# Performance work log

Measured on AMD Instinct MI355X. Metric: run time of the kernel, lower is better.

The kernel has to match this reference:

```python
import jax, jax.numpy as jnp
import numpy as np

B, S, D, H = 2, 2048, 1024, 16
HD = D // H  # head_dim = 64

def setup_inputs() -> dict:
    key = jax.random.key(0)
    ks = jax.random.split(key, 10)
    s = 1.0 / np.sqrt(D)
    return {
        "hidden_states": jax.random.normal(ks[0], (B, S, D), jnp.float32),
        "attention_mask": jnp.ones((B, S), jnp.float32),
        "q_w": jax.random.uniform(ks[1], (D, D), jnp.float32, -s, s),
        "q_b": jax.random.uniform(ks[2], (D,), jnp.float32, -s, s),
        "k_w": jax.random.uniform(ks[3], (D, D), jnp.float32, -s, s),
        "k_b": jax.random.uniform(ks[4], (D,), jnp.float32, -s, s),
        "v_w": jax.random.uniform(ks[5], (D, D), jnp.float32, -s, s),
        "v_b": jax.random.uniform(ks[6], (D,), jnp.float32, -s, s),
        "o_w": jax.random.uniform(ks[7], (D, D), jnp.float32, -s, s),
        "o_b": jax.random.uniform(ks[8], (D,), jnp.float32, -s, s),
    }

def reference(hidden_states, attention_mask, q_w, q_b, k_w, k_b, v_w, v_b, o_w, o_b):
    scale = HD ** -0.5
    # projections; torch Linear: x @ W^T + b. Here weights stored as (D, D) used directly.
    q = hidden_states @ q_w + q_b  # [B,S,D]
    k = hidden_states @ k_w + k_b
    v = hidden_states @ v_w + v_b
    # split heads -> [B,H,S,HD]
    q = q.reshape(B, S, H, HD).transpose(0, 2, 1, 3)
    k = k.reshape(B, S, H, HD).transpose(0, 2, 1, 3)
    v = v.reshape(B, S, H, HD).transpose(0, 2, 1, 3)
    scores = jnp.einsum('bhqd,bhkd->bhqk', q, k) * scale  # [B,H,S,S]
    # additive mask from 2D [B,S] mask (1=keep, 0=mask)
    scores = scores + (1.0 - attention_mask)[:, None, None, :] * -10000.0
    attn = jax.nn.softmax(scores, axis=-1)
    ctx = jnp.einsum('bhqk,bhkd->bhqd', attn, v)  # [B,H,S,HD]
    ctx = ctx.transpose(0, 2, 1, 3).reshape(B, S, D)
    return ctx @ o_w + o_b
```

## Files before the change

kernel.cpp:

```cpp
#include <hip/hip_runtime.h>
#include <hip/hip_bf16.h>

#define B_ 2
#define S_ 2048
#define D_ 1024
#define H_ 16
#define HD_ 64

#define QSCALE 0.18033688f
#define MLOG2E 14426.950408f

#define EXP2(x) __builtin_amdgcn_exp2f(x)

typedef __attribute__((ext_vector_type(8))) short bf16x8;
typedef __attribute__((ext_vector_type(4))) short short4v;
typedef __attribute__((ext_vector_type(4))) float floatx4;
typedef __attribute__((ext_vector_type(16))) float f32x16;

static __device__ __forceinline__ short f2bf(float f) {
  union { float f; unsigned int i; } c; c.f = f;
  unsigned int r = c.i + 0x7FFFu + ((c.i >> 16) & 1u);
  return (short)(r >> 16);
}

static __device__ __forceinline__ int cvtpk_bf16(float a, float b) {
  int r;
  asm("v_cvt_pk_bf16_f32 %0, %1, %2" : "=v"(r) : "v"(a), "v"(b));
  return r;
}
static __device__ __forceinline__ void swap32(int& a, int& b) {
  asm("v_permlane32_swap_b32 %0, %1" : "+v"(a), "+v"(b));
}

static __device__ __forceinline__ void gld_lds16(const void* g, void* l) {
  __builtin_amdgcn_global_load_lds(
      (const __attribute__((address_space(1))) unsigned int*)g,
      (__attribute__((address_space(3))) unsigned int*)l, 16, 0, 0);
}

__global__ __launch_bounds__(256)
void prep(const float* __restrict__ w0, const float* __restrict__ w1,
          const float* __restrict__ w2, const float* __restrict__ w3,
          const float* __restrict__ hs, short* __restrict__ WT,
          short* __restrict__ Xb) {
  const int z = blockIdx.z;
  if (z < 4) {
    __shared__ short t[64][65];
    const float* src = z == 0 ? w0 : z == 1 ? w1 : z == 2 ? w2 : w3;
    short* dst = WT + (size_t)z * D_ * D_;
    const int tx = threadIdx.x & 63, ty = threadIdx.x >> 6;
    const int r0 = blockIdx.y * 64, c0 = blockIdx.x * 64;
    for (int r = ty; r < 64; r += 4)
      t[r][tx] = f2bf(src[(size_t)(r0 + r) * D_ + c0 + tx]);
    __syncthreads();
    for (int r = ty; r < 64; r += 4)
      dst[(size_t)(c0 + r) * D_ + r0 + tx] = t[tx][r];
  } else {
    const int bid = blockIdx.y * 16 + blockIdx.x;
    const float4* in4 = (const float4*)hs;
    short4v* out4 = (short4v*)Xb;
#pragma unroll
    for (int i = 0; i < 16; i++) {
      const int idx = bid * 4096 + i * 256 + threadIdx.x;
      const float4 v = in4[idx];
      short4v o;
      o[0] = f2bf(v.x); o[1] = f2bf(v.y); o[2] = f2bf(v.z); o[3] = f2bf(v.w);
      out4[idx] = o;
    }
  }
}

__global__ __launch_bounds__(256, 2)
void gemm_qkv(const short* __restrict__ X, const short* __restrict__ WT,
              const float* __restrict__ qb, const float* __restrict__ kb,
              const float* __restrict__ vb,
              short* __restrict__ Qo, short* __restrict__ Ko,
              short* __restrict__ Vt) {
  __shared__ __align__(16) short As[128 * 32];
  __shared__ __align__(16) short Bs[128 * 32];
  const int tid = threadIdx.x;
  const int wave = tid >> 6, lane = tid & 63;
  const int col = lane & 15, quad = lane >> 4;
  const int m0 = blockIdx.x * 128;
  const int nt = blockIdx.y;
  const int widx = nt >> 3;
  const int n1 = (nt & 7) * 128;
  const short* Bsrc = WT + (size_t)widx * D_ * D_ + (size_t)n1 * D_;
  const int b = m0 >> 11;

  const int srow = tid >> 2;
  const int skcol = (tid & 3) * 8;
  const short* ga = X + (size_t)(m0 + srow) * D_ + skcol;
  const short* gb = Bsrc + (size_t)srow * D_ + skcol;
  short* la = As + tid * 8;
  short* lb = Bs + tid * 8;

  floatx4 acc[4][4];
#pragma unroll
  for (int i = 0; i < 4; i++)
#pragma unroll
    for (int j = 0; j < 4; j++) acc[i][j] = floatx4{0.f, 0.f, 0.f, 0.f};

  if (widx < 2) {
    const int wseq = (wave >> 1) * 64;
    const int wfeat = (wave & 1) * 64;
    for (int k0 = 0; k0 < D_; k0 += 32) {
      gld_lds16(ga, la);
      gld_lds16(ga + 64 * D_, la + 2048);
      gld_lds16(gb, lb);
      gld_lds16(gb + 64 * D_, lb + 2048);
      ga += 32; gb += 32;
      __syncthreads();
      bf16x8 xf[4], wf[4];
#pragma unroll
      for (int j = 0; j < 4; j++)
        xf[j] = *(const bf16x8*)(As + (wseq + j * 16 + col) * 32 + quad * 8);
#pragma unroll
      for (int i = 0; i < 4; i++)
        wf[i] = *(const bf16x8*)(Bs + (wfeat + i * 16 + col) * 32 + quad * 8);
#pragma unroll
      for (int i = 0; i < 4; i++)
#pragma unroll
        for (int j = 0; j < 4; j++)
          acc[i][j] = __builtin_amdgcn_mfma_f32_16x16x32_bf16(wf[i], xf[j],
                                                              acc[i][j], 0, 0, 0);
      __syncthreads();
    }
    const float* bias = widx == 0 ? qb : kb;
    short* dst = widx == 0 ? Qo : Ko;
    const float scale = widx == 0 ? QSCALE : 1.0f;
#pragma unroll
    for (int i = 0; i < 4; i++) {
      const int nf = n1 + wfeat + i * 16 + quad * 4;
      const int h = nf >> 6, hd = nf & 63;
      const float4 bv = *(const float4*)(bias + nf);
#pragma unroll
      for (int j = 0; j < 4; j++) {
        const int s = (m0 + wseq + j * 16 + col) & (S_ - 1);
        short4v pk;
        pk[0] = f2bf((acc[i][j][0] + bv.x) * scale);
        pk[1] = f2bf((acc[i][j][1] + bv.y) * scale);
        pk[2] = f2bf((acc[i][j][2] + bv.z) * scale);
        pk[3] = f2bf((acc[i][j][3] + bv.w) * scale);
        *(short4v*)(dst + ((size_t)(b * H_ + h) * S_ + s) * HD_ + hd) = pk;
      }
    }
  } else {
    const int wrow = (wave & 1) * 64;
    const int wcol = (wave >> 1) * 64;
    for (int k0 = 0; k0 < D_; k0 += 32) {
      gld_lds16(ga, la);
      gld_lds16(ga + 64 * D_, la + 2048);
      gld_lds16(gb, lb);
      gld_lds16(gb + 64 * D_, lb + 2048);
      ga += 32; gb += 32;
      __syncthreads();
      bf16x8 af[4], bfr[4];
#pragma unroll
      for (int i = 0; i < 4; i++)
        af[i] = *(const bf16x8*)(As + (wrow + i * 16 + col) * 32 + quad * 8);
#pragma unroll
      for (int j = 0; j < 4; j++)
        bfr[j] = *(const bf16x8*)(Bs + (wcol + j * 16 + col) * 32 + quad * 8);
#pragma unroll
      for (int i = 0; i < 4; i++)
#pragma unroll
        for (int j = 0; j < 4; j++)
          acc[i][j] = __builtin_amdgcn_mfma_f32_16x16x32_bf16(af[i], bfr[j],
                                                              acc[i][j], 0, 0, 0);
      __syncthreads();
    }
    float bv[4];
#pragma unroll
    for (int j = 0; j < 4; j++) bv[j] = vb[n1 + wcol + j * 16 + col];
#pragma unroll
    for (int i = 0; i < 4; i++) {
      const int s = (m0 + wrow + i * 16 + quad * 4) & (S_ - 1);
#pragma unroll
      for (int j = 0; j < 4; j++) {
        const int nl = n1 + wcol + j * 16 + col;
        const int h = nl >> 6, hd = nl & 63;
        short4v pk;
#pragma unroll
        for (int r = 0; r < 4; r++) pk[r] = f2bf(acc[i][j][r] + bv[j]);
        *(short4v*)(Vt + ((size_t)(b * H_ + h) * HD_ + hd) * S_ + s) = pk;
      }
    }
  }
}

__global__ __launch_bounds__(256, 4)
void attn(const short* __restrict__ Q, const short* __restrict__ K,
          const short* __restrict__ Vt, const float* __restrict__ mask,
          float* __restrict__ ctxP0, float* __restrict__ ctxP1,
          float* __restrict__ rsP0, float* __restrict__ rsP1) {
  __shared__ __align__(16) short Ks[2][4096];
  __shared__ __align__(16) short Vs[2][4096];
  __shared__ __align__(16) float Wb[1024];
  const int tid = threadIdx.x, wave = tid >> 6, lane = tid & 63;
  const int l31 = lane & 31, hi = lane >> 5, x7 = l31 & 7;
  const int lin = blockIdx.x;
  const int kh = (lin >> 3) & 1;
  const int qt = (lin >> 4) & 15;
  const int gi = (lin & 7) + ((lin >> 8) << 3);
  const int h = gi & 15, b = gi >> 4;
  const short* Qh = Q + (size_t)(b * H_ + h) * S_ * HD_;
  const short* Kh = K + (size_t)(b * H_ + h) * S_ * HD_;
  const short* Vh = Vt + (size_t)(b * H_ + h) * HD_ * S_;
  const float* mk = mask + (size_t)b * S_;
  const int q0 = qt * 128 + wave * 32;
  const int kk0 = kh * 1024;

  int srow[2], schk[2];
#pragma unroll
  for (int i = 0; i < 2; i++) {
    const int s = tid + i * 256;
    srow[i] = s >> 3;
    schk[i] = ((s & 7) ^ (srow[i] & 7)) * 8;
  }

#pragma unroll
  for (int i = 0; i < 2; i++) {
    gld_lds16(Kh + (size_t)(kk0 + srow[i]) * HD_ + schk[i],
              &Ks[0][(tid + i * 256) * 8]);
    gld_lds16(Vh + (size_t)srow[i] * S_ + kk0 + schk[i],
              &Vs[0][(tid + i * 256) * 8]);
  }

  for (int i = tid; i < 1024; i += 256)
    Wb[i] = (mk[kk0 + i] - 1.0f) * MLOG2E;

  bf16x8 qf[4];
  {
    const short* qp = Qh + (size_t)(q0 + l31) * HD_ + hi * 8;
#pragma unroll
    for (int c = 0; c < 4; c++) qf[c] = *(const bf16x8*)(qp + c * 16);
  }

  bf16x8 ones;
#pragma unroll
  for (int i = 0; i < 8; i++) ones[i] = (short)0x3F80;

  f32x16 acc0, acc1, rsa;
#pragma unroll
  for (int r = 0; r < 16; r++) { acc0[r] = 0.f; acc1[r] = 0.f; rsa[r] = 0.f; }

  const int kbase = l31 * 64;
  int ko[4];
#pragma unroll
  for (int c = 0; c < 4; c++) ko[c] = ((((c << 1) | hi) ^ x7) << 3);

  __syncthreads();

  for (int it = 0; it < 16; it++) {
    const int buf = it & 1;
    const int ktl = it * 64;
    if (it + 1 < 16) {
      const int kn = kk0 + ktl + 64;
#pragma unroll
      for (int i = 0; i < 2; i++) {
        gld_lds16(Kh + (size_t)(kn + srow[i]) * HD_ + schk[i],
                  &Ks[buf ^ 1][(tid + i * 256) * 8]);
        gld_lds16(Vh + (size_t)srow[i] * S_ + kn + schk[i],
                  &Vs[buf ^ 1][(tid + i * 256) * 8]);
      }
    }

    bf16x8 pB[4];
#pragma unroll
    for (int t = 0; t < 2; t++) {
      const int kb2 = ktl + t * 32 + 4 * hi;
      const float4 b0 = *(const float4*)&Wb[kb2];
      const float4 b1 = *(const float4*)&Wb[kb2 + 8];
      const float4 b2 = *(const float4*)&Wb[kb2 + 16];
      const float4 b3 = *(const float4*)&Wb[kb2 + 24];
      f32x16 z;
      z[0] = b0.x; z[1] = b0.y; z[2]  = b0.z; z[3]  = b0.w;
      z[4] = b1.x; z[5] = b1.y; z[6]  = b1.z; z[7]  = b1.w;
      z[8] = b2.x; z[9] = b2.y; z[10] = b2.z; z[11] = b2.w;
      z[12] = b3.x; z[13] = b3.y; z[14] = b3.z; z[15] = b3.w;
      const short* kp = &Ks[buf][t * 2048 + kbase];
      __builtin_amdgcn_s_setprio(1);
#pragma unroll
      for (int c = 0; c < 4; c++) {
        const bf16x8 kf = *(const bf16x8*)(kp + ko[c]);
        z = __builtin_amdgcn_mfma_f32_32x32x16_bf16(kf, qf[c], z, 0, 0, 0);
      }
      __builtin_amdgcn_s_setprio(0);
      float p[16];
#pragma unroll
      for (int r = 0; r < 16; r++) p[r] = EXP2(z[r]);
      int a0 = cvtpk_bf16(p[0], p[1]),   a1 = cvtpk_bf16(p[2], p[3]);
      int cc0 = cvtpk_bf16(p[4], p[5]),  cc1 = cvtpk_bf16(p[6], p[7]);
      int e0 = cvtpk_bf16(p[8], p[9]),   e1 = cvtpk_bf16(p[10], p[11]);
      int g0 = cvtpk_bf16(p[12], p[13]), g1 = cvtpk_bf16(p[14], p[15]);
      swap32(a0, cc0); swap32(a1, cc1);
      swap32(e0, g0);  swap32(e1, g1);
      union { int i[4]; bf16x8 v; } u0, u1;
      u0.i[0] = a0; u0.i[1] = a1; u0.i[2] = cc0; u0.i[3] = cc1;
      u1.i[0] = e0; u1.i[1] = e1; u1.i[2] = g0;  u1.i[3] = g1;
      pB[t * 2] = u0.v;
      pB[t * 2 + 1] = u1.v;
    }

    const short* vp0 = &Vs[buf][kbase];
    const short* vp1 = &Vs[buf][2048 + kbase];
    __builtin_amdgcn_s_setprio(1);
#pragma unroll
    for (int kc = 0; kc < 4; kc++)
      rsa = __builtin_amdgcn_mfma_f32_32x32x16_bf16(ones, pB[kc], rsa, 0, 0, 0);
#pragma unroll
    for (int kc = 0; kc < 4; kc++) {
      const bf16x8 vf0 = *(const bf16x8*)(vp0 + ko[kc]);
      const bf16x8 vf1 = *(const bf16x8*)(vp1 + ko[kc]);
      acc0 = __builtin_amdgcn_mfma_f32_32x32x16_bf16(vf0, pB[kc], acc0, 0, 0, 0);
      acc1 = __builtin_amdgcn_mfma_f32_32x32x16_bf16(vf1, pB[kc], acc1, 0, 0, 0);
    }
    __builtin_amdgcn_s_setprio(0);
    __syncthreads();
  }

  float* ctxP = kh ? ctxP1 : ctxP0;
  float* rsP  = kh ? rsP1  : rsP0;
  const size_t row = (size_t)b * S_ + q0 + l31;
#pragma unroll
  for (int g4 = 0; g4 < 4; g4++) {
    float* cp = ctxP + row * D_ + h * HD_ + g4 * 8 + 4 * hi;
    *(float4*)(cp) = make_float4(acc0[g4 * 4 + 0], acc0[g4 * 4 + 1],
                                 acc0[g4 * 4 + 2], acc0[g4 * 4 + 3]);
    *(float4*)(cp + 32) = make_float4(acc1[g4 * 4 + 0], acc1[g4 * 4 + 1],
                                      acc1[g4 * 4 + 2], acc1[g4 * 4 + 3]);
  }
  if (hi == 0)
    rsP[(size_t)(b * H_ + h) * S_ + q0 + l31] = rsa[0];
}

__global__ __launch_bounds__(256)
void combine(const float* __restrict__ P0, const float* __restrict__ P1,
             const float* __restrict__ rs0, const float* __restrict__ rs1,
             short* __restrict__ ctx) {
  const int t = blockIdx.x * 256 + threadIdx.x;
  const int row = t >> 7;
  const int dq = (t & 127) * 8;
  const int b = row >> 11, s = row & (S_ - 1);
  const int h = dq >> 6;
  const size_t base = (size_t)row * D_ + dq;
  const float4 a0 = *(const float4*)(P0 + base);
  const float4 a1 = *(const float4*)(P0 + base + 4);
  const float4 c0 = *(const float4*)(P1 + base);
  const float4 c1 = *(const float4*)(P1 + base + 4);
  const size_t ri = (size_t)(b * H_ + h) * S_ + s;
  const float inv = 1.0f / (rs0[ri] + rs1[ri] + 1e-30f);
  union { short sh[8]; int4 v; } o;
  o.sh[0] = f2bf((a0.x + c0.x) * inv);
  o.sh[1] = f2bf((a0.y + c0.y) * inv);
  o.sh[2] = f2bf((a0.z + c0.z) * inv);
  o.sh[3] = f2bf((a0.w + c0.w) * inv);
  o.sh[4] = f2bf((a1.x + c1.x) * inv);
  o.sh[5] = f2bf((a1.y + c1.y) * inv);
  o.sh[6] = f2bf((a1.z + c1.z) * inv);
  o.sh[7] = f2bf((a1.w + c1.w) * inv);
  *(int4*)(ctx + base) = o.v;
}

__global__ __launch_bounds__(256, 2)
void gemm_out(const short* __restrict__ X, const short* __restrict__ WT,
              const float* __restrict__ ob, float* __restrict__ out) {
  __shared__ __align__(16) short As[64 * 32];
  __shared__ __align__(16) short Bs[128 * 32];
  const int tid = threadIdx.x;
  const int wave = tid >> 6, lane = tid & 63;
  const int col = lane & 15, quad = lane >> 4;
  const int m0 = blockIdx.x * 64;
  const int n0 = blockIdx.y * 128;
  const short* Bsrc = WT + (size_t)n0 * D_;
  const int wrow = (wave & 1) * 32;
  const int wcol = (wave >> 1) * 64;

  floatx4 acc[2][4];
#pragma unroll
  for (int i = 0; i < 2; i++)
#pragma unroll
    for (int j = 0; j < 4; j++) acc[i][j] = floatx4{0.f, 0.f, 0.f, 0.f};

  const int arow = tid >> 2, akcol = (tid & 3) * 8;
  const short* ga = X + (size_t)(m0 + arow) * D_ + akcol;
  const short* gb = Bsrc + (size_t)arow * D_ + akcol;
  short* la = As + tid * 8;
  short* lb = Bs + tid * 8;

  for (int k0 = 0; k0 < D_; k0 += 32) {
    gld_lds16(ga, la);
    gld_lds16(gb, lb);
    gld_lds16(gb + 64 * D_, lb + 2048);
    ga += 32; gb += 32;
    __syncthreads();
    bf16x8 af[2], bfr[4];
#pragma unroll
    for (int i = 0; i < 2; i++)
      af[i] = *(const bf16x8*)(As + (wrow + i * 16 + col) * 32 + quad * 8);
#pragma unroll
    for (int j = 0; j < 4; j++)
      bfr[j] = *(const bf16x8*)(Bs + (wcol + j * 16 + col) * 32 + quad * 8);
#pragma unroll
    for (int i = 0; i < 2; i++)
#pragma unroll
      for (int j = 0; j < 4; j++)
        acc[i][j] = __builtin_amdgcn_mfma_f32_16x16x32_bf16(af[i], bfr[j],
                                                            acc[i][j], 0, 0, 0);
    __syncthreads();
  }

  float bv[4];
#pragma unroll
  for (int j = 0; j < 4; j++) bv[j] = ob[n0 + wcol + j * 16 + col];

#pragma unroll
  for (int i = 0; i < 2; i++) {
    const int m = m0 + wrow + i * 16 + quad * 4;
#pragma unroll
    for (int j = 0; j < 4; j++) {
      const int n = n0 + wcol + j * 16 + col;
#pragma unroll
      for (int r = 0; r < 4; r++)
        out[(size_t)(m + r) * D_ + n] = acc[i][j][r] + bv[j];
    }
  }
}

extern "C" void kernel_launch(void* const* d_in, const int* in_sizes, int n_in,
                              void* d_out, int out_size, void* d_ws, size_t ws_size,
                              hipStream_t stream) {
  (void)in_sizes; (void)n_in; (void)out_size; (void)ws_size;
  const float* hs  = (const float*)d_in[0];
  const float* msk = (const float*)d_in[1];
  const float* qw  = (const float*)d_in[2];
  const float* qb  = (const float*)d_in[3];
  const float* kw  = (const float*)d_in[4];
  const float* kb  = (const float*)d_in[5];
  const float* vw  = (const float*)d_in[6];
  const float* vb  = (const float*)d_in[7];
  const float* ow  = (const float*)d_in[8];
  const float* ob  = (const float*)d_in[9];
  float* out = (float*)d_out;
  char* ws = (char*)d_ws;

  short* Xb   = (short*)(ws);
  short* WT   = (short*)(ws + (8ull  << 20));
  short* Qp   = (short*)(ws + (16ull << 20));
  short* Kp   = (short*)(ws + (24ull << 20));
  short* Vtp  = (short*)(ws + (32ull << 20));
  float* ctxP0 = (float*)(ws + (40ull << 20));
  float* ctxP1 = (float*)(ws + (56ull << 20));
  float* rsP0  = (float*)(ws + (72ull << 20));
  float* rsP1  = (float*)(ws + (73ull << 20));
  short* Ctx  = Xb;

  prep<<<dim3(16, 16, 5), 256, 0, stream>>>(qw, kw, vw, ow, hs, WT, Xb);
  gemm_qkv<<<dim3(32, 24), 256, 0, stream>>>(Xb, WT, qb, kb, vb, Qp, Kp, Vtp);
  attn<<<dim3(1024), 256, 0, stream>>>(Qp, Kp, Vtp, msk, ctxP0, ctxP1, rsP0, rsP1);
  combine<<<dim3(2048), 256, 0, stream>>>(ctxP0, ctxP1, rsP0, rsP1, Ctx);
  gemm_out<<<dim3(64, 8), 256, 0, stream>>>(Ctx, WT + 3ull * D_ * D_, ob, out);
}
```

Baseline: 196.8 us.

## Process two 32-row query groups per wave in attention, halving block size

The attention kernel now uses 128-thread blocks where each wave handles 64 query rows (two 32-row groups) instead of 32. Each K and V fragment loaded from LDS is reused for two MFMA chains, halving LDS reads per FLOP. The PV accumulation is also interleaved per 32-key half-tile. The cost is doubled accumulator and Q-fragment register state, which lowers occupancy (launch bounds 128,2), and fewer waves per block to hide global-to-LDS load latency.

```diff
diff --git a/kernel.cpp b/kernel.cpp
--- a/kernel.cpp
+++ b/kernel.cpp
@@ -189,7 +189,7 @@
   }
 }
 
-__global__ __launch_bounds__(256, 4)
+__global__ __launch_bounds__(128, 2)
 void attn(const short* __restrict__ Q, const short* __restrict__ K,
           const short* __restrict__ Vt, const float* __restrict__ mask,
           float* __restrict__ ctxP0, float* __restrict__ ctxP1,
@@ -208,42 +208,45 @@
   const short* Kh = K + (size_t)(b * H_ + h) * S_ * HD_;
   const short* Vh = Vt + (size_t)(b * H_ + h) * HD_ * S_;
   const float* mk = mask + (size_t)b * S_;
-  const int q0 = qt * 128 + wave * 32;
+  const int q0 = qt * 128 + wave * 64;
   const int kk0 = kh * 1024;
 
-  int srow[2], schk[2];
-#pragma unroll
-  for (int i = 0; i < 2; i++) {
-    const int s = tid + i * 256;
+  int srow[4], schk[4];
+#pragma unroll
+  for (int i = 0; i < 4; i++) {
+    const int s = tid + i * 128;
     srow[i] = s >> 3;
     schk[i] = ((s & 7) ^ (srow[i] & 7)) * 8;
   }
 
 #pragma unroll
-  for (int i = 0; i < 2; i++) {
+  for (int i = 0; i < 4; i++) {
     gld_lds16(Kh + (size_t)(kk0 + srow[i]) * HD_ + schk[i],
-              &Ks[0][(tid + i * 256) * 8]);
+              &Ks[0][(tid + i * 128) * 8]);
     gld_lds16(Vh + (size_t)srow[i] * S_ + kk0 + schk[i],
-              &Vs[0][(tid + i * 256) * 8]);
-  }
-
-  for (int i = tid; i < 1024; i += 256)
+              &Vs[0][(tid + i * 128) * 8]);
+  }
+
+  for (int i = tid; i < 1024; i += 128)
     Wb[i] = (mk[kk0 + i] - 1.0f) * MLOG2E;
 
-  bf16x8 qf[4];
-  {
-    const short* qp = Qh + (size_t)(q0 + l31) * HD_ + hi * 8;
-#pragma unroll
-    for (int c = 0; c < 4; c++) qf[c] = *(const bf16x8*)(qp + c * 16);
+  bf16x8 qf[2][4];
+#pragma unroll
+  for (int g = 0; g < 2; g++) {
+    const short* qp = Qh + (size_t)(q0 + g * 32 + l31) * HD_ + hi * 8;
+#pragma unroll
+    for (int c = 0; c < 4; c++) qf[g][c] = *(const bf16x8*)(qp + c * 16);
   }
 
   bf16x8 ones;
 #pragma unroll
   for (int i = 0; i < 8; i++) ones[i] = (short)0x3F80;
 
-  f32x16 acc0, acc1, rsa;
-#pragma unroll
-  for (int r = 0; r < 16; r++) { acc0[r] = 0.f; acc1[r] = 0.f; rsa[r] = 0.f; }
+  f32x16 acc0[2], acc1[2], rsa[2];
+#pragma unroll
+  for (int g = 0; g < 2; g++)
+#pragma unroll
+    for (int r = 0; r < 16; r++) { acc0[g][r] = 0.f; acc1[g][r] = 0.f; rsa[g][r] = 0.f; }
 
   const int kbase = l31 * 64;
   int ko[4];
@@ -258,15 +261,14 @@
     if (it + 1 < 16) {
       const int kn = kk0 + ktl + 64;
 #pragma unroll
-      for (int i = 0; i < 2; i++) {
+      for (int i = 0; i < 4; i++) {
         gld_lds16(Kh + (size_t)(kn + srow[i]) * HD_ + schk[i],
-                  &Ks[buf ^ 1][(tid + i * 256) * 8]);
+                  &Ks[buf ^ 1][(tid + i * 128) * 8]);
         gld_lds16(Vh + (size_t)srow[i] * S_ + kn + schk[i],
-                  &Vs[buf ^ 1][(tid + i * 256) * 8]);
+                  &Vs[buf ^ 1][(tid + i * 128) * 8]);
       }
     }
 
-    bf16x8 pB[4];
 #pragma unroll
     for (int t = 0; t < 2; t++) {
       const int kb2 = ktl + t * 32 + 4 * hi;
@@ -274,65 +276,83 @@
       const float4 b1 = *(const float4*)&Wb[kb2 + 8];
       const float4 b2 = *(const float4*)&Wb[kb2 + 16];
       const float4 b3 = *(const float4*)&Wb[kb2 + 24];
-      f32x16 z;
-      z[0] = b0.x; z[1] = b0.y; z[2]  = b0.z; z[3]  = b0.w;
-      z[4] = b1.x; z[5] = b1.y; z[6]  = b1.z; z[7]  = b1.w;
-      z[8] = b2.x; z[9] = b2.y; z[10] = b2.z; z[11] = b2.w;
-      z[12] = b3.x; z[13] = b3.y; z[14] = b3.z; z[15] = b3.w;
+      f32x16 zs;
+      zs[0] = b0.x; zs[1] = b0.y; zs[2]  = b0.z; zs[3]  = b0.w;
+      zs[4] = b1.x; zs[5] = b1.y; zs[6]  = b1.z; zs[7]  = b1.w;
+      zs[8] = b2.x; zs[9] = b2.y; zs[10] = b2.z; zs[11] = b2.w;
+      zs[12] = b3.x; zs[13] = b3.y; zs[14] = b3.z; zs[15] = b3.w;
       const short* kp = &Ks[buf][t * 2048 + kbase];
+      bf16x8 kf[4];
+#pragma unroll
+      for (int c = 0; c < 4; c++) kf[c] = *(const bf16x8*)(kp + ko[c]);
+
+      bf16x8 pB[2][2];
+#pragma unroll
+      for (int g = 0; g < 2; g++) {
+        f32x16 z = zs;
+        __builtin_amdgcn_s_setprio(1);
+#pragma unroll
+        for (int c = 0; c < 4; c++)
+          z = __builtin_amdgcn_mfma_f32_32x32x16_bf16(kf[c], qf[g][c], z, 0, 0, 0);
+        __builtin_amdgcn_s_setprio(0);
+        float p[16];
+#pragma unroll
+        for (int r = 0; r < 16; r++) p[r] = EXP2(z[r]);
+        int a0 = cvtpk_bf16(p[0], p[1]),   a1 = cvtpk_bf16(p[2], p[3]);
+        int cc0 = cvtpk_bf16(p[4], p[5]),  cc1 = cvtpk_bf16(p[6], p[7]);
+        int e0 = cvtpk_bf16(p[8], p[9]),   e1 = cvtpk_bf16(p[10], p[11]);
+        int g0 = cvtpk_bf16(p[12], p[13]), g1 = cvtpk_bf16(p[14], p[15]);
+        swap32(a0, cc0); swap32(a1, cc1);
+        swap32(e0, g0);  swap32(e1, g1);
+        union { int i[4]; bf16x8 v; } u0, u1;
+        u0.i[0] = a0; u0.i[1] = a1; u0.i[2] = cc0; u0.i[3] = cc1;
+        u1.i[0] = e0; u1.i[1] = e1; u1.i[2] = g0;  u1.i[3] = g1;
+        pB[g][0] = u0.v;
+        pB[g][1] = u1.v;
+      }
+
+      const short* vp0 = &Vs[buf][kbase];
+      const short* vp1 = &Vs[buf][2048 + kbase];
+      bf16x8 vA[2], vB[2];
+#pragma unroll
+      for (int u = 0; u < 2; u++) {
+        vA[u] = *(const bf16x8*)(vp0 + ko[2 * t + u]);
+        vB[u] = *(const bf16x8*)(vp1 + ko[2 * t + u]);
+      }
       __builtin_amdgcn_s_setprio(1);
 #pragma unroll
-      for (int c = 0; c < 4; c++) {
-        const bf16x8 kf = *(const bf16x8*)(kp + ko[c]);
-        z = __builtin_amdgcn_mfma_f32_32x32x16_bf16(kf, qf[c], z, 0, 0, 0);
-      }
+      for (int g = 0; g < 2; g++)
+#pragma unroll
+        for (int u = 0; u < 2; u++)
+          rsa[g] = __builtin_amdgcn_mfma_f32_32x32x16_bf16(ones, pB[g][u], rsa[g], 0, 0, 0);
+#pragma unroll
+      for (int g = 0; g < 2; g++)
+#pragma unroll
+        for (int u = 0; u < 2; u++) {
+          acc0[g] = __builtin_amdgcn_mfma_f32_32x32x16_bf16(vA[u], pB[g][u], acc0[g], 0, 0, 0);
+          acc1[g] = __builtin_amdgcn_mfma_f32_32x32x16_bf16(vB[u], pB[g][u], acc1[g], 0, 0, 0);
+        }
       __builtin_amdgcn_s_setprio(0);
-      float p[16];
-#pragma unroll
-      for (int r = 0; r < 16; r++) p[r] = EXP2(z[r]);
-      int a0 = cvtpk_bf16(p[0], p[1]),   a1 = cvtpk_bf16(p[2], p[3]);
-      int cc0 = cvtpk_bf16(p[4], p[5]),  cc1 = cvtpk_bf16(p[6], p[7]);
-      int e0 = cvtpk_bf16(p[8], p[9]),   e1 = cvtpk_bf16(p[10], p[11]);
-      int g0 = cvtpk_bf16(p[12], p[13]), g1 = cvtpk_bf16(p[14], p[15]);
-      swap32(a0, cc0); swap32(a1, cc1);
-      swap32(e0, g0);  swap32(e1, g1);
-      union { int i[4]; bf16x8 v; } u0, u1;
-      u0.i[0] = a0; u0.i[1] = a1; u0.i[2] = cc0; u0.i[3] = cc1;
-      u1.i[0] = e0; u1.i[1] = e1; u1.i[2] = g0;  u1.i[3] = g1;
-      pB[t * 2] = u0.v;
-      pB[t * 2 + 1] = u1.v;
-    }
-
-    const short* vp0 = &Vs[buf][kbase];
-    const short* vp1 = &Vs[buf][2048 + kbase];
-    __builtin_amdgcn_s_setprio(1);
-#pragma unroll
-    for (int kc = 0; kc < 4; kc++)
-      rsa = __builtin_amdgcn_mfma_f32_32x32x16_bf16(ones, pB[kc], rsa, 0, 0, 0);
-#pragma unroll
-    for (int kc = 0; kc < 4; kc++) {
-      const bf16x8 vf0 = *(const bf16x8*)(vp0 + ko[kc]);
-      const bf16x8 vf1 = *(const bf16x8*)(vp1 + ko[kc]);
-      acc0 = __builtin_amdgcn_mfma_f32_32x32x16_bf16(vf0, pB[kc], acc0, 0, 0, 0);
-      acc1 = __builtin_amdgcn_mfma_f32_32x32x16_bf16(vf1, pB[kc], acc1, 0, 0, 0);
-    }
-    __builtin_amdgcn_s_setprio(0);
+    }
     __syncthreads();
   }
 
   float* ctxP = kh ? ctxP1 : ctxP0;
   float* rsP  = kh ? rsP1  : rsP0;
-  const size_t row = (size_t)b * S_ + q0 + l31;
-#pragma unroll
-  for (int g4 = 0; g4 < 4; g4++) {
-    float* cp = ctxP + row * D_ + h * HD_ + g4 * 8 + 4 * hi;
-    *(float4*)(cp) = make_float4(acc0[g4 * 4 + 0], acc0[g4 * 4 + 1],
-                                 acc0[g4 * 4 + 2], acc0[g4 * 4 + 3]);
-    *(float4*)(cp + 32) = make_float4(acc1[g4 * 4 + 0], acc1[g4 * 4 + 1],
-                                      acc1[g4 * 4 + 2], acc1[g4 * 4 + 3]);
-  }
-  if (hi == 0)
-    rsP[(size_t)(b * H_ + h) * S_ + q0 + l31] = rsa[0];
+#pragma unroll
+  for (int g = 0; g < 2; g++) {
+    const size_t row = (size_t)b * S_ + q0 + g * 32 + l31;
+#pragma unroll
+    for (int g4 = 0; g4 < 4; g4++) {
+      float* cp = ctxP + row * D_ + h * HD_ + g4 * 8 + 4 * hi;
+      *(float4*)(cp) = make_float4(acc0[g][g4 * 4 + 0], acc0[g][g4 * 4 + 1],
+                                   acc0[g][g4 * 4 + 2], acc0[g][g4 * 4 + 3]);
+      *(float4*)(cp + 32) = make_float4(acc1[g][g4 * 4 + 0], acc1[g][g4 * 4 + 1],
+                                        acc1[g][g4 * 4 + 2], acc1[g][g4 * 4 + 3]);
+    }
+    if (hi == 0)
+      rsP[(size_t)(b * H_ + h) * S_ + q0 + g * 32 + l31] = rsa[g][0];
+  }
 }
 
 __global__ __launch_bounds__(256)
@@ -458,7 +478,7 @@
 
   prep<<<dim3(16, 16, 5), 256, 0, stream>>>(qw, kw, vw, ow, hs, WT, Xb);
   gemm_qkv<<<dim3(32, 24), 256, 0, stream>>>(Xb, WT, qb, kb, vb, Qp, Kp, Vtp);
-  attn<<<dim3(1024), 256, 0, stream>>>(Qp, Kp, Vtp, msk, ctxP0, ctxP1, rsP0, rsP1);
+  attn<<<dim3(1024), 128, 0, stream>>>(Qp, Kp, Vtp, msk, ctxP0, ctxP1, rsP0, rsP1);
   combine<<<dim3(2048), 256, 0, stream>>>(ctxP0, ctxP1, rsP0, rsP1, Ctx);
   gemm_out<<<dim3(64, 8), 256, 0, stream>>>(Ctx, WT + 3ull * D_ * D_, ob, out);
 }
```

Measured after the change: 200.9 us. +2.0%, slower.
